# Kernel optimization log

Hardware: AMD Instinct MI355X
Metric: run time of the kernel (lower is better)

The kernel has to match this reference:

```python
import jax, jax.numpy as jnp
import numpy as np

N = 100000   # nodes
E = 1600000  # edges
NC = 10000   # candidates
G = 1000     # graphs
ND = 32      # node_emb_dim
ED = 8       # edge_emb_dim
L = 4        # num_layers


def setup_inputs() -> dict:
    key = jax.random.key(0)
    ks = jax.random.split(key, 12)
    s = 0.1
    return {
        "x": jax.random.normal(ks[0], (N, 2), dtype=jnp.float32),
        "edge_attr": jax.random.normal(ks[1], (E, 1), dtype=jnp.float32),
        "Wn_in": jax.random.normal(ks[2], (2, ND)) * s,
        "bn_in": jnp.zeros((ND,)),
        "We_in": jax.random.normal(ks[3], (1, ED)) * s,
        "be_in": jnp.zeros((ED,)),
        "We_l": jax.random.normal(ks[4], (L, 2 * ND + ED, ED)) * s,
        "be_l": jnp.zeros((L, ED)),
        "Wn_l": jax.random.normal(ks[5], (L, ND + ED, ND)) * s,
        "bn_l": jnp.zeros((L, ND)),
        "Wout": jax.random.normal(ks[6], (ND, 1)) * s,
        "bout": jnp.zeros((1,)),
        "edge_index": jax.random.randint(ks[7], (2, E), 0, N),
        "batch": jnp.sort(jax.random.randint(ks[8], (N,), 0, G)),
        "candidate_idxs": jax.random.randint(ks[9], (NC,), 0, N),
    }


def reference(x, edge_attr, Wn_in, bn_in, We_in, be_in, We_l, be_l, Wn_l, bn_l,
              Wout, bout, edge_index, batch, candidate_idxs):
    h = x @ Wn_in + bn_in            # [N, ND]
    e = edge_attr @ We_in + be_in    # [E, ED]
    src, dst = edge_index[0], edge_index[1]
    for l in range(L):
        # edge update: MLP on [x_src, x_dst, edge_attr]
        m = jnp.concatenate([h[src], h[dst], e], axis=-1)        # [E, 2*ND+ED]
        new_e = jax.nn.relu(m @ We_l[l] + be_l[l])               # [E, ED]
        # aggregate (aggr='add') messages at destination nodes
        agg = jax.ops.segment_sum(new_e, dst, num_segments=N)    # [N, ED]
        new_h = jax.nn.relu(jnp.concatenate([h, agg], axis=-1) @ Wn_l[l] + bn_l[l])
        h = h + new_h   # residual
        e = e + new_e   # residual
    logits = (h[candidate_idxs] @ Wout + bout)[:, 0]             # [NC]
    seg = batch[candidate_idxs]                                  # [NC] graph ids
    # scatter_log_softmax over per-graph candidate groups
    mx = jax.ops.segment_max(logits, seg, num_segments=G)
    shifted = logits - mx[seg]
    lse = jnp.log(jax.ops.segment_sum(jnp.exp(shifted), seg, num_segments=G))
    return shifted - lse[seg]
```

## Files before the change

kernel.cpp:

```cpp
#include <hip/hip_runtime.h>

#define ND 32
#define ED 8
#define NL 4
#define NG 1000
#define NBC_MAX 512
#define CHUNK 8192
#define CHUNK_H 4096

typedef unsigned short u16;


__device__ __forceinline__ u16 f2bf(float f) {
  unsigned u = __float_as_uint(f);
  u += 0x7fffu + ((u >> 16) & 1u);
  return (u16)(u >> 16);
}
__device__ __forceinline__ unsigned pack2(float a, float b) {
  return (unsigned)f2bf(a) | ((unsigned)f2bf(b) << 16);
}
__device__ __forceinline__ void cvt8(uint4 p, float* o) {
  o[0] = __uint_as_float(p.x << 16); o[1] = __uint_as_float(p.x & 0xffff0000u);
  o[2] = __uint_as_float(p.y << 16); o[3] = __uint_as_float(p.y & 0xffff0000u);
  o[4] = __uint_as_float(p.z << 16); o[5] = __uint_as_float(p.z & 0xffff0000u);
  o[6] = __uint_as_float(p.w << 16); o[7] = __uint_as_float(p.w & 0xffff0000u);
}
__device__ __forceinline__ uint4 pack8(const float* v) {
  uint4 o;
  o.x = pack2(v[0], v[1]); o.y = pack2(v[2], v[3]);
  o.z = pack2(v[4], v[5]); o.w = pack2(v[6], v[7]);
  return o;
}


__global__ void k_init_h(const float* __restrict__ x,
                         const float* __restrict__ W,
                         const float* __restrict__ b,
                         const float* __restrict__ We,
                         const float* __restrict__ be,
                         u16* __restrict__ h,
                         u16* __restrict__ zs, u16* __restrict__ zd,
                         int N) {
  int n = blockIdx.x * blockDim.x + threadIdx.x;
  if (n >= N) return;
  float x0 = x[2 * n], x1 = x[2 * n + 1];
  float v[ND];
#pragma unroll
  for (int d = 0; d < ND; ++d) v[d] = fmaf(x0, W[d], fmaf(x1, W[ND + d], b[d]));
#pragma unroll
  for (int d = 0; d < ND; ++d) v[d] = __uint_as_float((unsigned)f2bf(v[d]) << 16);
  uint4* h4 = reinterpret_cast<uint4*>(h + (size_t)n * ND);
#pragma unroll
  for (int q = 0; q < 4; ++q) h4[q] = pack8(&v[q * 8]);
  float zsv[ED], zdv[ED];
#pragma unroll
  for (int j = 0; j < ED; ++j) { zsv[j] = 0.0f; zdv[j] = be[j]; }
#pragma unroll
  for (int k = 0; k < ND; ++k)
#pragma unroll
    for (int j = 0; j < ED; ++j) {
      zsv[j] = fmaf(v[k], We[k * ED + j], zsv[j]);
      zdv[j] = fmaf(v[k], We[(ND + k) * ED + j], zdv[j]);
    }
  *reinterpret_cast<uint4*>(zs + (size_t)n * ED) = pack8(zsv);
  *reinterpret_cast<uint4*>(zd + (size_t)n * ED) = pack8(zdv);
}


__global__ void k_chist(const int* __restrict__ dst, int* __restrict__ bcnt,
                        int E, int nbc) {
  __shared__ int lcnt[NBC_MAX];
  for (int b = threadIdx.x; b < nbc; b += blockDim.x) lcnt[b] = 0;
  __syncthreads();
  int e0 = blockIdx.x * CHUNK_H;
  int e1 = min(e0 + CHUNK_H, E);
  for (int i = e0 + threadIdx.x; i < e1; i += blockDim.x)
    atomicAdd(&lcnt[dst[i] >> 8], 1);
  __syncthreads();
  for (int b = threadIdx.x; b < nbc; b += blockDim.x)
    if (lcnt[b]) atomicAdd(&bcnt[b], lcnt[b]);
}

__global__ void k_cscan(const int* __restrict__ bcnt, int* __restrict__ bbase,
                        int nbc) {
  __shared__ int s[NBC_MAX];
  int tid = threadIdx.x;
  if (nbc <= NBC_MAX) {
    int v = (tid < nbc) ? bcnt[tid] : 0;
    s[tid] = v;
    __syncthreads();
    for (int st = 1; st < NBC_MAX; st <<= 1) {
      int t = (tid >= st) ? s[tid - st] : 0;
      __syncthreads();
      s[tid] += t;
      __syncthreads();
    }
    if (tid < nbc) bbase[tid] = s[tid] - v;
    if (tid == nbc - 1) bbase[nbc] = s[tid];
  } else if (tid == 0) {
    int run = 0;
    for (int i = 0; i < nbc; ++i) { bbase[i] = run; run += bcnt[i]; }
    bbase[nbc] = run;
  }
}

__global__ void k_binA(const int* __restrict__ src, const int* __restrict__ dst,
                       const float* __restrict__ ea,
                       const int* __restrict__ bbase, int* __restrict__ cursor_c,
                       int4* __restrict__ binned, int E, int nbc) {
  __shared__ int lcnt[NBC_MAX];
  __shared__ int lbase[NBC_MAX];
  for (int b = threadIdx.x; b < nbc; b += blockDim.x) lcnt[b] = 0;
  __syncthreads();
  int e0 = blockIdx.x * CHUNK;
  int e1 = min(e0 + CHUNK, E);
  for (int i = e0 + threadIdx.x; i < e1; i += blockDim.x)
    atomicAdd(&lcnt[dst[i] >> 8], 1);
  __syncthreads();
  for (int b = threadIdx.x; b < nbc; b += blockDim.x) {
    int c = lcnt[b];
    lbase[b] = c ? (bbase[b] + atomicAdd(&cursor_c[b], c)) : 0;
  }
  __syncthreads();
  for (int i = e0 + threadIdx.x; i < e1; i += blockDim.x) {
    int d = dst[i];
    int pos = atomicAdd(&lbase[d >> 8], 1);
    binned[pos] = make_int4(src[i], d, __float_as_int(ea[i]), 0);
  }
}

__global__ void k_binB(const int4* __restrict__ binned,
                       const int* __restrict__ bbase,
                       uint2* __restrict__ sedge, u16* __restrict__ e,
                       int* __restrict__ noffs,
                       const float* __restrict__ We,
                       const float* __restrict__ be,
                       int N) {
  __shared__ int hist[256];
  __shared__ int scn[256];
  int b = blockIdx.x;
  int base = bbase[b], end = bbase[b + 1];
  int node0 = b << 8;
  int nn = min(256, N - node0);
  hist[threadIdx.x] = 0;
  __syncthreads();
  for (int p = base + threadIdx.x; p < end; p += blockDim.x)
    atomicAdd(&hist[binned[p].y & 255], 1);
  __syncthreads();
  int v = hist[threadIdx.x];
  scn[threadIdx.x] = v;
  __syncthreads();
  for (int st = 1; st < 256; st <<= 1) {
    int t = (threadIdx.x >= (unsigned)st) ? scn[threadIdx.x - st] : 0;
    __syncthreads();
    scn[threadIdx.x] += t;
    __syncthreads();
  }
  int excl = base + scn[threadIdx.x] - v;
  if ((int)threadIdx.x < nn) noffs[node0 + threadIdx.x] = excl;
  if (threadIdx.x == 0) noffs[min(node0 + 256, N)] = end;
  hist[threadIdx.x] = excl;
  __syncthreads();
  for (int p = base + threadIdx.x; p < end; p += blockDim.x) {
    int4 rec = binned[p];
    int pos = atomicAdd(&hist[rec.y & 255], 1);
    sedge[pos] = make_uint2((unsigned)rec.x, (unsigned)rec.y);
    float a = __int_as_float(rec.z);
    float e0[ED];
#pragma unroll
    for (int j = 0; j < ED; ++j) e0[j] = fmaf(a, We[j], be[j]);
    *reinterpret_cast<uint4*>(e + (size_t)pos * ED) = pack8(e0);
  }
}


template <bool LAST>
__global__ void k_edge(const u16* __restrict__ zs,
                       const u16* __restrict__ zd,
                       u16* __restrict__ e,
                       u16* __restrict__ ne,
                       const uint2* __restrict__ sedge,
                       const float* __restrict__ W3,
                       int E) {
  int nb = gridDim.x;
  int per = nb >> 3;
  int b = blockIdx.x;
  int lb = (b < (per << 3)) ? ((b & 7) * per + (b >> 3)) : b;
  int i = lb * blockDim.x + threadIdx.x;
  if (i >= E) return;
  uint2 sd = sedge[i];
  float zsv[ED], zdv[ED], ein[ED], acc[ED];
  cvt8(*reinterpret_cast<const uint4*>(zs + (size_t)sd.x * ED), zsv);
  cvt8(*reinterpret_cast<const uint4*>(zd + (size_t)sd.y * ED), zdv);
  cvt8(*reinterpret_cast<const uint4*>(e + (size_t)i * ED), ein);
#pragma unroll
  for (int j = 0; j < ED; ++j) acc[j] = zsv[j] + zdv[j];
#pragma unroll
  for (int k = 0; k < ED; ++k)
#pragma unroll
    for (int j = 0; j < ED; ++j)
      acc[j] = fmaf(ein[k], W3[k * ED + j], acc[j]);
#pragma unroll
  for (int j = 0; j < ED; ++j) acc[j] = fmaxf(acc[j], 0.0f);
  *reinterpret_cast<uint4*>(ne + (size_t)i * ED) = pack8(acc);
  if (!LAST) {
    float eo[ED];
#pragma unroll
    for (int j = 0; j < ED; ++j) eo[j] = ein[j] + acc[j];
    *reinterpret_cast<uint4*>(e + (size_t)i * ED) = pack8(eo);
  }
}

template <bool PROJ>
__global__ void k_node(u16* __restrict__ h,
                       const u16* __restrict__ ne,
                       const int* __restrict__ noffs,
                       const float* __restrict__ W,
                       const float* __restrict__ b,
                       const float* __restrict__ Wen,
                       const float* __restrict__ ben,
                       u16* __restrict__ zs, u16* __restrict__ zd,
                       int N) {
  int n = blockIdx.x * blockDim.x + threadIdx.x;
  if (n >= N) return;
  int o0 = noffs[n], o1 = noffs[n + 1];
  float av[ED];
#pragma unroll
  for (int j = 0; j < ED; ++j) av[j] = 0.0f;
  for (int p = o0; p < o1; ++p) {
    float t[ED];
    cvt8(*reinterpret_cast<const uint4*>(ne + (size_t)p * ED), t);
#pragma unroll
    for (int j = 0; j < ED; ++j) av[j] += t[j];
  }
  float acc[ND];
#pragma unroll
  for (int j = 0; j < ND; ++j) acc[j] = b[j];
  uint4* h4 = reinterpret_cast<uint4*>(h + (size_t)n * ND);
  float hv[ND];
#pragma unroll
  for (int q = 0; q < 4; ++q) cvt8(h4[q], &hv[q * 8]);
#pragma unroll
  for (int k = 0; k < ND; ++k)
#pragma unroll
    for (int j = 0; j < ND; ++j) acc[j] = fmaf(hv[k], W[k * ND + j], acc[j]);
#pragma unroll
  for (int k = 0; k < ED; ++k)
#pragma unroll
    for (int j = 0; j < ND; ++j) acc[j] = fmaf(av[k], W[(ND + k) * ND + j], acc[j]);
  float hn[ND];
#pragma unroll
  for (int k = 0; k < ND; ++k) {
    float o = hv[k] + fmaxf(acc[k], 0.0f);
    hn[k] = __uint_as_float((unsigned)f2bf(o) << 16);
  }
#pragma unroll
  for (int q = 0; q < 4; ++q) h4[q] = pack8(&hn[q * 8]);
  if (PROJ) {
    float zsv[ED], zdv[ED];
#pragma unroll
    for (int j = 0; j < ED; ++j) { zsv[j] = 0.0f; zdv[j] = ben[j]; }
#pragma unroll
    for (int k = 0; k < ND; ++k)
#pragma unroll
      for (int j = 0; j < ED; ++j) {
        zsv[j] = fmaf(hn[k], Wen[k * ED + j], zsv[j]);
        zdv[j] = fmaf(hn[k], Wen[(ND + k) * ED + j], zdv[j]);
      }
    *reinterpret_cast<uint4*>(zs + (size_t)n * ED) = pack8(zsv);
    *reinterpret_cast<uint4*>(zd + (size_t)n * ED) = pack8(zdv);
  }
}


__device__ __forceinline__ unsigned int enc_f32(float f) {
  unsigned int bits = __float_as_uint(f);
  return (bits & 0x80000000u) ? ~bits : (bits | 0x80000000u);
}
__device__ __forceinline__ float dec_f32(unsigned int u) {
  unsigned int bits = (u & 0x80000000u) ? (u ^ 0x80000000u) : ~u;
  return __uint_as_float(bits);
}

__global__ void k_logits(const u16* __restrict__ h,
                         const int* __restrict__ cand,
                         const int* __restrict__ batch,
                         const float* __restrict__ Wout,
                         const float* __restrict__ bout,
                         float* __restrict__ logits,
                         int* __restrict__ seg,
                         unsigned int* __restrict__ mxu,
                         int NC) {
  int c = blockIdx.x * blockDim.x + threadIdx.x;
  if (c >= NC) return;
  int idx = cand[c];
  const uint4* hr = reinterpret_cast<const uint4*>(h + (size_t)idx * ND);
  float acc = bout[0];
  float v[8];
#pragma unroll
  for (int q = 0; q < 4; ++q) {
    cvt8(hr[q], v);
#pragma unroll
    for (int k = 0; k < 8; ++k) acc = fmaf(v[k], Wout[q * 8 + k], acc);
  }
  logits[c] = acc;
  int g = batch[idx];
  seg[c] = g;
  atomicMax(&mxu[g], enc_f32(acc));
}

__global__ void k_expsum(float* __restrict__ logits,
                         const int* __restrict__ seg,
                         const unsigned int* __restrict__ mxu,
                         float* __restrict__ sum,
                         int NC) {
  int c = blockIdx.x * blockDim.x + threadIdx.x;
  if (c >= NC) return;
  int g = seg[c];
  float sh = logits[c] - dec_f32(mxu[g]);
  logits[c] = sh;
  atomicAdd(&sum[g], expf(sh));
}

__global__ void k_final(const float* __restrict__ shifted,
                        const int* __restrict__ seg,
                        const float* __restrict__ sum,
                        float* __restrict__ out, int NC) {
  int c = blockIdx.x * blockDim.x + threadIdx.x;
  if (c >= NC) return;
  out[c] = shifted[c] - logf(sum[seg[c]]);
}


extern "C" void kernel_launch(void* const* d_in, const int* in_sizes, int n_in,
                              void* d_out, int out_size, void* d_ws, size_t ws_size,
                              hipStream_t stream) {
  const float* x       = (const float*)d_in[0];
  const float* ea      = (const float*)d_in[1];
  const float* Wn_in   = (const float*)d_in[2];
  const float* bn_in   = (const float*)d_in[3];
  const float* We_in   = (const float*)d_in[4];
  const float* be_in   = (const float*)d_in[5];
  const float* We_l    = (const float*)d_in[6];
  const float* be_l    = (const float*)d_in[7];
  const float* Wn_l    = (const float*)d_in[8];
  const float* bn_l    = (const float*)d_in[9];
  const float* Wout    = (const float*)d_in[10];
  const float* bout    = (const float*)d_in[11];
  const int* edge_index= (const int*)d_in[12];
  const int* batch     = (const int*)d_in[13];
  const int* cand      = (const int*)d_in[14];

  const int N  = in_sizes[13];
  const int E  = in_sizes[1];
  const int NC = in_sizes[14];
  const int nbc = (N + 255) >> 8;

  char* ws = (char*)d_ws;
  int4*  binned = (int4*)ws;  ws += (size_t)E * sizeof(int4);
  uint2* sedge  = (uint2*)ws; ws += (size_t)E * sizeof(uint2);
  u16*   h      = (u16*)ws;   ws += (size_t)N * ND * sizeof(u16);
  u16*   e      = (u16*)ws;   ws += (size_t)E * ED * sizeof(u16);
  u16*   ne     = (u16*)ws;   ws += (size_t)E * ED * sizeof(u16);
  u16*   zs     = (u16*)ws;   ws += (size_t)N * ED * sizeof(u16);
  u16*   zd     = (u16*)ws;   ws += (size_t)N * ED * sizeof(u16);
  int*   noffs  = (int*)ws;   ws += ((size_t)N + 4) * sizeof(int);
  int*   bcnt   = (int*)ws;   ws += (size_t)NBC_MAX * sizeof(int);
  int*   cursor = (int*)ws;   ws += (size_t)NBC_MAX * sizeof(int);
  int*   bbase  = (int*)ws;   ws += ((size_t)NBC_MAX + 4) * sizeof(int);
  float* logits = (float*)ws; ws += (size_t)NC * sizeof(float);
  int*   seg    = (int*)ws;   ws += (size_t)NC * sizeof(int);
  unsigned int* mxu = (unsigned int*)ws; ws += (size_t)NG * sizeof(unsigned int);
  float* sum    = (float*)ws; ws += (size_t)NG * sizeof(float);

  const int* srcp = edge_index;
  const int* dstp = edge_index + E;
  const int blk = 256;
  const size_t WE_STRIDE = (size_t)(2 * ND + ED) * ED;

  hipMemsetAsync(bcnt, 0, (size_t)NBC_MAX * sizeof(int), stream);
  hipMemsetAsync(cursor, 0, (size_t)NBC_MAX * sizeof(int), stream);
  k_chist<<<(E + CHUNK_H - 1) / CHUNK_H, 1024, 0, stream>>>(dstp, bcnt, E, nbc);
  k_cscan<<<1, NBC_MAX, 0, stream>>>(bcnt, bbase, nbc);
  k_binA<<<(E + CHUNK - 1) / CHUNK, 1024, 0, stream>>>(srcp, dstp, ea, bbase,
                                                       cursor, binned, E, nbc);
  k_binB<<<nbc, 256, 0, stream>>>(binned, bbase, sedge, e, noffs, We_in, be_in, N);

  k_init_h<<<(N + blk - 1) / blk, blk, 0, stream>>>(x, Wn_in, bn_in, We_l, be_l,
                                                    h, zs, zd, N);

  for (int l = 0; l < NL; ++l) {
    const float* W3 = We_l + l * WE_STRIDE + (size_t)2 * ND * ED;
    if (l + 1 < NL) {
      k_edge<false><<<(E + blk - 1) / blk, blk, 0, stream>>>(zs, zd, e, ne,
                                                             sedge, W3, E);
      k_node<true><<<(N + blk - 1) / blk, blk, 0, stream>>>(
          h, ne, noffs, Wn_l + (size_t)l * (ND + ED) * ND, bn_l + (size_t)l * ND,
          We_l + (l + 1) * WE_STRIDE, be_l + (size_t)(l + 1) * ED, zs, zd, N);
    } else {
      k_edge<true><<<(E + blk - 1) / blk, blk, 0, stream>>>(zs, zd, e, ne,
                                                            sedge, W3, E);
      k_node<false><<<(N + blk - 1) / blk, blk, 0, stream>>>(
          h, ne, noffs, Wn_l + (size_t)l * (ND + ED) * ND, bn_l + (size_t)l * ND,
          nullptr, nullptr, nullptr, nullptr, N);
    }
  }

  hipMemsetAsync(mxu, 0, NG * sizeof(unsigned int), stream);
  hipMemsetAsync(sum, 0, NG * sizeof(float), stream);
  k_logits<<<(NC + blk - 1) / blk, blk, 0, stream>>>(h, cand, batch, Wout, bout,
                                                     logits, seg, mxu, NC);
  k_expsum<<<(NC + blk - 1) / blk, blk, 0, stream>>>(logits, seg, mxu, sum, NC);
  k_final<<<(NC + blk - 1) / blk, blk, 0, stream>>>(logits, seg, sum,
                                                    (float*)d_out, NC);
}
```

Measured before the change: 367.7 us.

## Fuse edge update and node aggregation into one per-node layer kernel

Merges the per-edge update kernel and the per-node aggregation kernel into one kernel where each node thread walks its dst-sorted incoming edges, computes the edge MLP, accumulates the messages and updates its node. This removes the ne buffer write and re-read and halves the per-layer launches. Projected zs/zd buffers are double-buffered to avoid read/write races, and adjacent memsets are merged. The trade-off is that the edge work is now serialized per node thread with degree imbalance and less parallelism (N threads instead of E).

```diff
diff --git a/kernel.cpp b/kernel.cpp
--- a/kernel.cpp
+++ b/kernel.cpp
@@ -131,7 +131,7 @@
 
 __global__ void k_binB(const int4* __restrict__ binned,
                        const int* __restrict__ bbase,
-                       uint2* __restrict__ sedge, u16* __restrict__ e,
+                       int* __restrict__ ssrc, u16* __restrict__ e,
                        int* __restrict__ noffs,
                        const float* __restrict__ We,
                        const float* __restrict__ be,
@@ -164,7 +164,7 @@
   for (int p = base + threadIdx.x; p < end; p += blockDim.x) {
     int4 rec = binned[p];
     int pos = atomicAdd(&hist[rec.y & 255], 1);
-    sedge[pos] = make_uint2((unsigned)rec.x, (unsigned)rec.y);
+    ssrc[pos] = rec.x;
     float a = __int_as_float(rec.z);
     float e0[ED];
 #pragma unroll
@@ -173,69 +173,55 @@
   }
 }
 
-
 template <bool LAST>
-__global__ void k_edge(const u16* __restrict__ zs,
-                       const u16* __restrict__ zd,
-                       u16* __restrict__ e,
-                       u16* __restrict__ ne,
-                       const uint2* __restrict__ sedge,
-                       const float* __restrict__ W3,
-                       int E) {
-  int nb = gridDim.x;
-  int per = nb >> 3;
-  int b = blockIdx.x;
-  int lb = (b < (per << 3)) ? ((b & 7) * per + (b >> 3)) : b;
-  int i = lb * blockDim.x + threadIdx.x;
-  if (i >= E) return;
-  uint2 sd = sedge[i];
-  float zsv[ED], zdv[ED], ein[ED], acc[ED];
-  cvt8(*reinterpret_cast<const uint4*>(zs + (size_t)sd.x * ED), zsv);
-  cvt8(*reinterpret_cast<const uint4*>(zd + (size_t)sd.y * ED), zdv);
-  cvt8(*reinterpret_cast<const uint4*>(e + (size_t)i * ED), ein);
-#pragma unroll
-  for (int j = 0; j < ED; ++j) acc[j] = zsv[j] + zdv[j];
-#pragma unroll
-  for (int k = 0; k < ED; ++k)
-#pragma unroll
-    for (int j = 0; j < ED; ++j)
-      acc[j] = fmaf(ein[k], W3[k * ED + j], acc[j]);
-#pragma unroll
-  for (int j = 0; j < ED; ++j) acc[j] = fmaxf(acc[j], 0.0f);
-  *reinterpret_cast<uint4*>(ne + (size_t)i * ED) = pack8(acc);
-  if (!LAST) {
-    float eo[ED];
-#pragma unroll
-    for (int j = 0; j < ED; ++j) eo[j] = ein[j] + acc[j];
-    *reinterpret_cast<uint4*>(e + (size_t)i * ED) = pack8(eo);
-  }
-}
-
-template <bool PROJ>
-__global__ void k_node(u16* __restrict__ h,
-                       const u16* __restrict__ ne,
-                       const int* __restrict__ noffs,
-                       const float* __restrict__ W,
-                       const float* __restrict__ b,
-                       const float* __restrict__ Wen,
-                       const float* __restrict__ ben,
-                       u16* __restrict__ zs, u16* __restrict__ zd,
-                       int N) {
+__global__ void k_layer(u16* __restrict__ h,
+                        const u16* __restrict__ zs_in,
+                        const u16* __restrict__ zd_in,
+                        u16* __restrict__ zs_out, u16* __restrict__ zd_out,
+                        u16* __restrict__ e,
+                        const int* __restrict__ ssrc,
+                        const int* __restrict__ noffs,
+                        const float* __restrict__ W3,
+                        const float* __restrict__ Wn,
+                        const float* __restrict__ bn,
+                        const float* __restrict__ Wen,
+                        const float* __restrict__ ben,
+                        int N) {
   int n = blockIdx.x * blockDim.x + threadIdx.x;
   if (n >= N) return;
   int o0 = noffs[n], o1 = noffs[n + 1];
+  float zdv[ED];
+  cvt8(*reinterpret_cast<const uint4*>(zd_in + (size_t)n * ED), zdv);
   float av[ED];
 #pragma unroll
   for (int j = 0; j < ED; ++j) av[j] = 0.0f;
   for (int p = o0; p < o1; ++p) {
-    float t[ED];
-    cvt8(*reinterpret_cast<const uint4*>(ne + (size_t)p * ED), t);
-#pragma unroll
-    for (int j = 0; j < ED; ++j) av[j] += t[j];
+    int s = ssrc[p];
+    float zsv[ED], ein[ED], acc[ED];
+    cvt8(*reinterpret_cast<const uint4*>(zs_in + (size_t)s * ED), zsv);
+    cvt8(*reinterpret_cast<const uint4*>(e + (size_t)p * ED), ein);
+#pragma unroll
+    for (int j = 0; j < ED; ++j) acc[j] = zsv[j] + zdv[j];
+#pragma unroll
+    for (int k = 0; k < ED; ++k)
+#pragma unroll
+      for (int j = 0; j < ED; ++j)
+        acc[j] = fmaf(ein[k], W3[k * ED + j], acc[j]);
+#pragma unroll
+    for (int j = 0; j < ED; ++j) {
+      acc[j] = fmaxf(acc[j], 0.0f);
+      av[j] += acc[j];
+    }
+    if (!LAST) {
+      float eo[ED];
+#pragma unroll
+      for (int j = 0; j < ED; ++j) eo[j] = ein[j] + acc[j];
+      *reinterpret_cast<uint4*>(e + (size_t)p * ED) = pack8(eo);
+    }
   }
   float acc[ND];
 #pragma unroll
-  for (int j = 0; j < ND; ++j) acc[j] = b[j];
+  for (int j = 0; j < ND; ++j) acc[j] = bn[j];
   uint4* h4 = reinterpret_cast<uint4*>(h + (size_t)n * ND);
   float hv[ND];
 #pragma unroll
@@ -243,11 +229,12 @@
 #pragma unroll
   for (int k = 0; k < ND; ++k)
 #pragma unroll
-    for (int j = 0; j < ND; ++j) acc[j] = fmaf(hv[k], W[k * ND + j], acc[j]);
+    for (int j = 0; j < ND; ++j) acc[j] = fmaf(hv[k], Wn[k * ND + j], acc[j]);
 #pragma unroll
   for (int k = 0; k < ED; ++k)
 #pragma unroll
-    for (int j = 0; j < ND; ++j) acc[j] = fmaf(av[k], W[(ND + k) * ND + j], acc[j]);
+    for (int j = 0; j < ND; ++j)
+      acc[j] = fmaf(av[k], Wn[(ND + k) * ND + j], acc[j]);
   float hn[ND];
 #pragma unroll
   for (int k = 0; k < ND; ++k) {
@@ -256,19 +243,19 @@
   }
 #pragma unroll
   for (int q = 0; q < 4; ++q) h4[q] = pack8(&hn[q * 8]);
-  if (PROJ) {
-    float zsv[ED], zdv[ED];
-#pragma unroll
-    for (int j = 0; j < ED; ++j) { zsv[j] = 0.0f; zdv[j] = ben[j]; }
+  if (!LAST) {
+    float zsv[ED], zdn[ED];
+#pragma unroll
+    for (int j = 0; j < ED; ++j) { zsv[j] = 0.0f; zdn[j] = ben[j]; }
 #pragma unroll
     for (int k = 0; k < ND; ++k)
 #pragma unroll
       for (int j = 0; j < ED; ++j) {
         zsv[j] = fmaf(hn[k], Wen[k * ED + j], zsv[j]);
-        zdv[j] = fmaf(hn[k], Wen[(ND + k) * ED + j], zdv[j]);
+        zdn[j] = fmaf(hn[k], Wen[(ND + k) * ED + j], zdn[j]);
       }
-    *reinterpret_cast<uint4*>(zs + (size_t)n * ED) = pack8(zsv);
-    *reinterpret_cast<uint4*>(zd + (size_t)n * ED) = pack8(zdv);
+    *reinterpret_cast<uint4*>(zs_out + (size_t)n * ED) = pack8(zsv);
+    *reinterpret_cast<uint4*>(zd_out + (size_t)n * ED) = pack8(zdn);
   }
 }
 
@@ -358,12 +345,13 @@
 
   char* ws = (char*)d_ws;
   int4*  binned = (int4*)ws;  ws += (size_t)E * sizeof(int4);
-  uint2* sedge  = (uint2*)ws; ws += (size_t)E * sizeof(uint2);
+  int*   ssrc   = (int*)ws;   ws += (size_t)E * sizeof(int);
   u16*   h      = (u16*)ws;   ws += (size_t)N * ND * sizeof(u16);
   u16*   e      = (u16*)ws;   ws += (size_t)E * ED * sizeof(u16);
-  u16*   ne     = (u16*)ws;   ws += (size_t)E * ED * sizeof(u16);
-  u16*   zs     = (u16*)ws;   ws += (size_t)N * ED * sizeof(u16);
-  u16*   zd     = (u16*)ws;   ws += (size_t)N * ED * sizeof(u16);
+  u16*   zsA    = (u16*)ws;   ws += (size_t)N * ED * sizeof(u16);
+  u16*   zdA    = (u16*)ws;   ws += (size_t)N * ED * sizeof(u16);
+  u16*   zsB    = (u16*)ws;   ws += (size_t)N * ED * sizeof(u16);
+  u16*   zdB    = (u16*)ws;   ws += (size_t)N * ED * sizeof(u16);
   int*   noffs  = (int*)ws;   ws += ((size_t)N + 4) * sizeof(int);
   int*   bcnt   = (int*)ws;   ws += (size_t)NBC_MAX * sizeof(int);
   int*   cursor = (int*)ws;   ws += (size_t)NBC_MAX * sizeof(int);
@@ -378,36 +366,36 @@
   const int blk = 256;
   const size_t WE_STRIDE = (size_t)(2 * ND + ED) * ED;
 
-  hipMemsetAsync(bcnt, 0, (size_t)NBC_MAX * sizeof(int), stream);
-  hipMemsetAsync(cursor, 0, (size_t)NBC_MAX * sizeof(int), stream);
+  hipMemsetAsync(bcnt, 0, 2 * (size_t)NBC_MAX * sizeof(int), stream);
   k_chist<<<(E + CHUNK_H - 1) / CHUNK_H, 1024, 0, stream>>>(dstp, bcnt, E, nbc);
   k_cscan<<<1, NBC_MAX, 0, stream>>>(bcnt, bbase, nbc);
   k_binA<<<(E + CHUNK - 1) / CHUNK, 1024, 0, stream>>>(srcp, dstp, ea, bbase,
                                                        cursor, binned, E, nbc);
-  k_binB<<<nbc, 256, 0, stream>>>(binned, bbase, sedge, e, noffs, We_in, be_in, N);
+  k_binB<<<nbc, 256, 0, stream>>>(binned, bbase, ssrc, e, noffs, We_in, be_in, N);
 
   k_init_h<<<(N + blk - 1) / blk, blk, 0, stream>>>(x, Wn_in, bn_in, We_l, be_l,
-                                                    h, zs, zd, N);
-
+                                                    h, zsA, zdA, N);
+
+  u16* zi[2] = {zsA, zsB};
+  u16* zj[2] = {zdA, zdB};
+  const int ngrid = (N + blk - 1) / blk;
   for (int l = 0; l < NL; ++l) {
     const float* W3 = We_l + l * WE_STRIDE + (size_t)2 * ND * ED;
+    const float* Wn = Wn_l + (size_t)l * (ND + ED) * ND;
+    const float* bn = bn_l + (size_t)l * ND;
+    int a = l & 1, b2 = (l + 1) & 1;
     if (l + 1 < NL) {
-      k_edge<false><<<(E + blk - 1) / blk, blk, 0, stream>>>(zs, zd, e, ne,
-                                                             sedge, W3, E);
-      k_node<true><<<(N + blk - 1) / blk, blk, 0, stream>>>(
-          h, ne, noffs, Wn_l + (size_t)l * (ND + ED) * ND, bn_l + (size_t)l * ND,
-          We_l + (l + 1) * WE_STRIDE, be_l + (size_t)(l + 1) * ED, zs, zd, N);
+      k_layer<false><<<ngrid, blk, 0, stream>>>(
+          h, zi[a], zj[a], zi[b2], zj[b2], e, ssrc, noffs, W3, Wn, bn,
+          We_l + (l + 1) * WE_STRIDE, be_l + (size_t)(l + 1) * ED, N);
     } else {
-      k_edge<true><<<(E + blk - 1) / blk, blk, 0, stream>>>(zs, zd, e, ne,
-                                                            sedge, W3, E);
-      k_node<false><<<(N + blk - 1) / blk, blk, 0, stream>>>(
-          h, ne, noffs, Wn_l + (size_t)l * (ND + ED) * ND, bn_l + (size_t)l * ND,
-          nullptr, nullptr, nullptr, nullptr, N);
+      k_layer<true><<<ngrid, blk, 0, stream>>>(
+          h, zi[a], zj[a], nullptr, nullptr, e, ssrc, noffs, W3, Wn, bn,
+          nullptr, nullptr, N);
     }
   }
 
-  hipMemsetAsync(mxu, 0, NG * sizeof(unsigned int), stream);
-  hipMemsetAsync(sum, 0, NG * sizeof(float), stream);
+  hipMemsetAsync(mxu, 0, NG * (sizeof(unsigned int) + sizeof(float)), stream);
   k_logits<<<(NC + blk - 1) / blk, blk, 0, stream>>>(h, cand, batch, Wout, bout,
                                                      logits, seg, mxu, NC);
   k_expsum<<<(NC + blk - 1) / blk, blk, 0, stream>>>(logits, seg, mxu, sum, NC);
```

After: 394.6 us. 1.07x slower.
